# Kernel optimization log

Measured on AMD Instinct MI355X. Metric: run time of the kernel, lower is better.

## Reference

```python
import jax, jax.numpy as jnp
import numpy as np

D_MODEL = 272
D_STATE = 32
N_LAYERS = 12
D_INNER = 2 * D_MODEL      # expand=2 (mamba_ssm default)
D_CONV = 4                 # mamba_ssm default
DT_RANK = (D_MODEL + 15) // 16  # ceil(272/16) = 17
B_SZ = 2
SEQ = 512


def setup_inputs() -> dict:
    key = jax.random.key(0)
    ks = jax.random.split(key, 16)
    rn = lambda k, shape, s=0.02: jax.random.normal(k, shape, jnp.float32) * s
    # dt bias init: softplus^{-1} of dt in [1e-3, 0.1] (mamba-style)
    dt0 = jax.random.uniform(ks[6], (N_LAYERS, 2, D_INNER), jnp.float32, 1e-3, 0.1)
    a_log = jnp.broadcast_to(jnp.log(jnp.arange(1, D_STATE + 1, dtype=jnp.float32)),
                             (N_LAYERS, 2, D_INNER, D_STATE))
    return {
        "x": jax.random.normal(ks[0], (B_SZ, SEQ, D_MODEL), jnp.float32),
        "y": jax.random.uniform(ks[1], (B_SZ, 1), jnp.float32),
        "in_proj_w": rn(ks[2], (N_LAYERS, 2, 2 * D_INNER, D_MODEL)),
        "conv_w": rn(ks[3], (N_LAYERS, 2, D_INNER, D_CONV), 0.1),
        "conv_b": jnp.zeros((N_LAYERS, 2, D_INNER), jnp.float32),
        "x_proj_w": rn(ks[4], (N_LAYERS, 2, DT_RANK + 2 * D_STATE, D_INNER)),
        "dt_proj_w": rn(ks[5], (N_LAYERS, 2, D_INNER, DT_RANK), 0.1),
        "dt_proj_b": jnp.log(jnp.expm1(dt0)),
        "A_log": a_log,
        "Dskip": jnp.ones((N_LAYERS, 2, D_INNER), jnp.float32),
        "out_proj_w": rn(ks[7], (N_LAYERS, 2, D_MODEL, D_INNER)),
        "lambda_q1": rn(ks[8], (N_LAYERS, D_MODEL), 0.05),
        "norm1_w": jnp.ones((N_LAYERS, D_MODEL), jnp.float32),
        "norm2_w": jnp.ones((N_LAYERS, D_MODEL), jnp.float32),
        "mlp_w": rn(ks[9], (D_MODEL, D_MODEL)),
        "mlp_b": jnp.zeros((D_MODEL,), jnp.float32),
        "predict_w": rn(ks[10], (1, D_MODEL + 1)),
        "predict_b": jnp.zeros((1,), jnp.float32),
    }


def _rmsnorm(x, w, eps=1e-5):
    return x * jax.lax.rsqrt(jnp.mean(x * x, axis=-1, keepdims=True) + eps) * w


def _mamba(x, p):
    """Single-direction Mamba block. x: (B, L, D_MODEL)."""
    in_w, cw, cb, xw, dtw, dtb, a_log, dskip, ow = p
    bsz = x.shape[0]
    xz = jnp.einsum('bld,ed->ble', x, in_w)            # (B,L,2*D_INNER)
    xin, z = jnp.split(xz, 2, axis=-1)
    # causal depthwise conv1d, kernel 4
    xc = jax.lax.conv_general_dilated(
        xin.transpose(0, 2, 1), cw[:, None, :], (1,), [(D_CONV - 1, 0)],
        feature_group_count=D_INNER, dimension_numbers=('NCL', 'OIL', 'NCL'))
    xc = jax.nn.silu(xc + cb[:, None]).transpose(0, 2, 1)  # (B,L,D_INNER)
    dbc = jnp.einsum('bld,ed->ble', xc, xw)
    dt, Bm, Cm = jnp.split(dbc, [DT_RANK, DT_RANK + D_STATE], axis=-1)
    dt = jax.nn.softplus(jnp.einsum('blr,dr->bld', dt, dtw) + dtb)  # (B,L,D_INNER)
    A = -jnp.exp(a_log)                                  # (D_INNER, D_STATE)

    @jax.checkpoint
    def step(h, inp):
        dt_t, x_t, B_t, C_t = inp                        # (B,Din),(B,Din),(B,Ds),(B,Ds)
        h = jnp.exp(dt_t[..., None] * A) * h + (dt_t * x_t)[..., None] * B_t[:, None, :]
        return h, jnp.einsum('bds,bs->bd', h, C_t)

    h0 = jnp.zeros((bsz, D_INNER, D_STATE), x.dtype)
    xs = (dt.transpose(1, 0, 2), xc.transpose(1, 0, 2),
          Bm.transpose(1, 0, 2), Cm.transpose(1, 0, 2))
    _, ys = jax.lax.scan(step, h0, xs)                   # ys: (L,B,D_INNER)
    yo = ys.transpose(1, 0, 2) + dskip * xc
    yo = yo * jax.nn.silu(z)
    return jnp.einsum('bld,od->blo', yo, ow)


def _forward(x, y, in_proj_w, conv_w, conv_b, x_proj_w, dt_proj_w, dt_proj_b,
             A_log, Dskip, out_proj_w, lambda_q1, norm1_w, norm2_w,
             mlp_w, mlp_b, predict_w, predict_b):
    mats = (in_proj_w, conv_w, conv_b, x_proj_w, dt_proj_w, dt_proj_b, A_log, Dskip, out_proj_w)
    for i in range(N_LAYERS):
        lam_init = 0.8 - 0.6 * np.exp(-0.3 * i)
        xn = _rmsnorm(x, norm1_w[i])
        lam_full = jax.nn.sigmoid(jnp.sum(lambda_q1[i])) + lam_init
        y1 = _mamba(xn, tuple(a[i, 0] for a in mats))
        y2 = jnp.flip(_mamba(jnp.flip(xn, 1), tuple(a[i, 1] for a in mats)), 1)
        attn = _rmsnorm(y1 - lam_full * y2, norm2_w[i])
        x = x + attn * (1.0 - lam_init)
    x2 = jax.nn.relu(jnp.mean(x, axis=1) @ mlp_w.T + mlp_b)
    feats = jnp.concatenate([x2, y], axis=-1)
    logits = feats @ predict_w.T + predict_b
    return logits, x2


def reference(x, y, in_proj_w, conv_w, conv_b, x_proj_w, dt_proj_w, dt_proj_b,
              A_log, Dskip, out_proj_w, lambda_q1, norm1_w, norm2_w,
              mlp_w, mlp_b, predict_w, predict_b):
    return _forward(x, y, in_proj_w, conv_w, conv_b, x_proj_w, dt_proj_w, dt_proj_b,
                    A_log, Dskip, out_proj_w, lambda_q1, norm1_w, norm2_w,
                    mlp_w, mlp_b, predict_w, predict_b)
```

## Files before the change

kernel.cpp:

```cpp
#include <hip/hip_runtime.h>
#include <math.h>

#define DM   272
#define DS   32
#define DI   544
#define DTR  17
#define SEQL 512
#define NB   2
#define ROWS 1024
#define DXZ  1088
#define NL   12
#define KP   288

typedef unsigned short ushort_t;
typedef __attribute__((ext_vector_type(8))) short bx8;
typedef __attribute__((ext_vector_type(4))) float fx4;

#define OFF_X     0
#define OFF_XZ    279552
#define OFF_XCT   2507776
#define OFF_DTT   3621888
#define OFF_ZT    4736000
#define OFF_BM    5850112
#define OFF_CM    5915648
#define OFF_YOT   5981184
#define OFF_Y12   7095296
#define OFF_XMP   7652352
#define OFF_DTWT  7656704
#define OFF_XNH   7878656
#define OFF_XNL   8026112
#define OFF_WINH  8173568
#define OFF_WINL  11933696
#define OFF_WOUTH 15693824
#define OFF_WOUTL 17469440

#define NINW  (12*2176*KP)
#define NOUTW (12*544*544)

__device__ __forceinline__ float sigmoid_fast(float x){ return 1.f/(1.f+__expf(-x)); }
__device__ __forceinline__ float softplus_f(float x){ return (x > 20.f) ? x : log1pf(__expf(x)); }

__device__ __forceinline__ void bf16split(float x, ushort_t& h, ushort_t& l){
  unsigned uh = __float_as_uint(x) & 0xffff0000u;
  h = (ushort_t)(uh >> 16);
  float r = x - __uint_as_float(uh);
  l = (ushort_t)(__float_as_uint(r) >> 16);
}

__device__ __forceinline__ float block_reduce_256(float v, volatile float* sred, int tid){
#pragma unroll
  for (int m=32; m>=1; m>>=1) v += __shfl_xor(v, m);
  __syncthreads();
  if ((tid & 63) == 0) sred[tid>>6] = v;
  __syncthreads();
  return sred[0]+sred[1]+sred[2]+sred[3];
}

__global__ __launch_bounds__(256) void k_prep(
    const float* __restrict__ inw, const float* __restrict__ outw,
    const float* __restrict__ dtw, const float* __restrict__ x0,
    const float* __restrict__ n1w0,
    ushort_t* __restrict__ winh, ushort_t* __restrict__ winl,
    ushort_t* __restrict__ wouth, ushort_t* __restrict__ woutl,
    float* __restrict__ dtwT, float* __restrict__ xb,
    ushort_t* __restrict__ xnh, ushort_t* __restrict__ xnl)
{
  const int bid = blockIdx.x, tid = threadIdx.x;
  for (int idx = bid*256 + tid; idx < NINW + NOUTW; idx += 1024*256){
    if (idx < NINW){
      int k = idx % KP; int row = idx / KP;
      float v = (k < DM) ? inw[(size_t)row*DM + k] : 0.f;
      ushort_t h,l; bf16split(v,h,l);
      winh[idx]=h; winl[idx]=l;
    } else {
      int j = idx - NINW;
      float v = outw[j];
      ushort_t h,l; bf16split(v,h,l);
      wouth[j]=h; woutl[j]=l;
    }
  }
  for (int idx = bid*256 + tid; idx < 24*544*DTR; idx += 1024*256){
    int ld = idx / (544*DTR); int rem = idx - ld*(544*DTR);
    int d = rem / DTR; int r = rem - d*DTR;
    dtwT[(size_t)ld*DTR*544 + (size_t)r*544 + d] = dtw[idx];
  }
  if (tid < 64){
    const int r = bid, l = tid;
    float vv[5]; float ss = 0.f;
#pragma unroll
    for (int i=0;i<5;i++){
      int c = l + i*64; float v = 0.f;
      if (c < DM){ v = x0[(size_t)r*DM+c]; xb[(size_t)r*DM+c]=v; }
      vv[i]=v; ss += v*v;
    }
#pragma unroll
    for (int m=32;m>=1;m>>=1) ss += __shfl_xor(ss,m);
    float ivr = rsqrtf(ss*(1.f/DM)+1e-5f);
#pragma unroll
    for (int i=0;i<5;i++){
      int c = l + i*64;
      if (c < DM){
        ushort_t h,lo; bf16split(vv[i]*ivr*n1w0[c],h,lo);
        xnh[(size_t)r*KP+c]=h; xnl[(size_t)r*KP+c]=lo;
      }
    }
    if (l < 16){ xnh[(size_t)r*KP+DM+l]=0; xnl[(size_t)r*KP+DM+l]=0; }
  }
}

__global__ __launch_bounds__(256) void k_gin(
  const ushort_t* __restrict__ xnh, const ushort_t* __restrict__ xnl,
  const ushort_t* __restrict__ wh,  const ushort_t* __restrict__ wl,
  float* __restrict__ xz)
{
  const int tid = threadIdx.x;
  const int wv = tid >> 6, lane = tid & 63;
  const int m16 = lane & 15, quad = lane >> 4;
  const int q8 = quad << 3;
  const int m0 = blockIdx.x << 6;
  const int nt = blockIdx.y;
  const int dir = (nt >= 17) ? 1 : 0;
  const int n0l = (nt - dir*17) << 6;
  const int ncol = n0l + (wv<<4) + m16;
  const ushort_t* bhp = wh + (size_t)(dir*1088 + ncol)*KP + q8;
  const ushort_t* blp = wl + (size_t)(dir*1088 + ncol)*KP + q8;
  const ushort_t* ahp = xnh + (size_t)(m0 + m16)*KP + q8;
  const ushort_t* alp = xnl + (size_t)(m0 + m16)*KP + q8;
  fx4 acc[4];
#pragma unroll
  for (int mt=0;mt<4;mt++) acc[mt] = (fx4){0.f,0.f,0.f,0.f};
  for (int k0=0;k0<KP;k0+=32){
    bx8 bh = *(const bx8*)(bhp + k0);
    bx8 bl = *(const bx8*)(blp + k0);
#pragma unroll
    for (int mt=0;mt<4;mt++){
      bx8 ah = *(const bx8*)(ahp + (size_t)mt*16*KP + k0);
      bx8 al = *(const bx8*)(alp + (size_t)mt*16*KP + k0);
      acc[mt] = __builtin_amdgcn_mfma_f32_16x16x32_bf16(ah, bh, acc[mt], 0,0,0);
      acc[mt] = __builtin_amdgcn_mfma_f32_16x16x32_bf16(al, bh, acc[mt], 0,0,0);
      acc[mt] = __builtin_amdgcn_mfma_f32_16x16x32_bf16(ah, bl, acc[mt], 0,0,0);
    }
  }
#pragma unroll
  for (int mt=0;mt<4;mt++){
#pragma unroll
    for (int r=0;r<4;r++){
      int rg = m0 + mt*16 + quad*4 + r;
      int b = rg >> 9, t = rg & 511;
      int ts = dir ? (511 - t) : t;
      xz[((size_t)((dir*NB + b)*SEQL + ts))*DXZ + ncol] = acc[mt][r];
    }
  }
}

__global__ __launch_bounds__(512) void k_xdt(
  const float* __restrict__ xz, const float* __restrict__ cwl, const float* __restrict__ cbl,
  const float* __restrict__ xwl, const float* __restrict__ dtwTl, const float* __restrict__ dtbl,
  float* __restrict__ xcT, float* __restrict__ dtT, float* __restrict__ zT,
  float* __restrict__ Bmg, float* __restrict__ Cmg)
{
  __shared__ float xcs[8][548];
  __shared__ float part[8][8][82];
  __shared__ float dts[8][DTR];
  const int tid = threadIdx.x;
  const int blk = blockIdx.x;
  const int seg = blk >> 6;
  const int dir = seg >> 1;
  const int t0 = (blk & 63) << 3;
  const float* xzb  = xz + (size_t)seg*SEQL*DXZ;
  const float* cw   = cwl + dir*DI*4;
  const float* cb   = cbl + dir*DI;
  const float* xw   = xwl + (size_t)dir*81*DI;
  const float* dtwT = dtwTl + (size_t)dir*DTR*DI;
  const float* dtb  = dtbl + dir*DI;
  const size_t chb = (size_t)seg*DI;

  for (int j = tid; j < DI; j += 512){
    float4 w4 = *(const float4*)(cw + j*4);
    float bj = cb[j];
    float xv[11];
#pragma unroll
    for (int q=0; q<11; q++){
      int t = t0 + q - 3;
      xv[q] = (t >= 0) ? xzb[(size_t)t*DXZ + j] : 0.f;
    }
    float xo[8], zo[8];
#pragma unroll
    for (int rr=0; rr<8; rr++){
      float acc = bj + w4.x*xv[rr] + w4.y*xv[rr+1] + w4.z*xv[rr+2] + w4.w*xv[rr+3];
      float v = acc * sigmoid_fast(acc);
      xcs[rr][j] = v; xo[rr] = v;
      zo[rr] = xzb[(size_t)(t0+rr)*DXZ + 544 + j];
    }
    float* xr = xcT + (chb + j)*SEQL + t0;
    *(float4*)(xr)   = make_float4(xo[0],xo[1],xo[2],xo[3]);
    *(float4*)(xr+4) = make_float4(xo[4],xo[5],xo[6],xo[7]);
    float* zr = zT + (chb + j)*SEQL + t0;
    *(float4*)(zr)   = make_float4(zo[0],zo[1],zo[2],zo[3]);
    *(float4*)(zr+4) = make_float4(zo[4],zo[5],zo[6],zo[7]);
  }
  __syncthreads();

  if (tid < 328){
    const int i = tid >> 3, ks = tid & 7;
    const int e0 = 2*i;
    const int e1r = (e0+1 < 81) ? (e0+1) : 80;
    const int kb = ks*68;
    const float* w0 = xw + (size_t)e0*DI + kb;
    const float* w1 = xw + (size_t)e1r*DI + kb;
    float acc0[8], acc1[8];
#pragma unroll
    for (int rr=0; rr<8; rr++){ acc0[rr]=0.f; acc1[rr]=0.f; }
    for (int k=0; k<68; k+=4){
      float4 wa = *(const float4*)(w0 + k);
      float4 wb = *(const float4*)(w1 + k);
#pragma unroll
      for (int rr=0; rr<8; rr++){
        float4 x4 = *(const float4*)(&xcs[rr][kb + k]);
        acc0[rr] = fmaf(wa.x,x4.x, fmaf(wa.y,x4.y, fmaf(wa.z,x4.z, fmaf(wa.w,x4.w, acc0[rr]))));
        acc1[rr] = fmaf(wb.x,x4.x, fmaf(wb.y,x4.y, fmaf(wb.z,x4.z, fmaf(wb.w,x4.w, acc1[rr]))));
      }
    }
#pragma unroll
    for (int rr=0; rr<8; rr++){
      part[ks][rr][e0]   = acc0[rr];
      part[ks][rr][e0+1] = acc1[rr];
    }
  }
  __syncthreads();

  for (int idx=tid; idx<648; idx+=512){
    int ta = idx / 81, e = idx - ta*81;
    float s = 0.f;
#pragma unroll
    for (int ks=0; ks<8; ks++) s += part[ks][ta][e];
    size_t row = (size_t)seg*SEQL + t0 + ta;
    if (e < DTR)      dts[ta][e] = s;
    else if (e < 49)  Bmg[row*DS + (e-DTR)] = s;
    else              Cmg[row*DS + (e-49)] = s;
  }
  __syncthreads();

  {
    const int c1 = tid;
    const bool h2 = tid < 32; const int c2 = 512 + tid;
    float w1[DTR], w2[DTR];
#pragma unroll
    for (int q=0; q<DTR; q++){
      w1[q] = dtwT[q*DI + c1];
      w2[q] = h2 ? dtwT[q*DI + c2] : 0.f;
    }
    float b1 = dtb[c1], b2 = h2 ? dtb[c2] : 0.f;
    float o1[8], o2[8];
#pragma unroll
    for (int rr=0; rr<8; rr++){
      float a1=b1, a2=b2;
#pragma unroll
      for (int q=0; q<DTR; q++){
        float dv = dts[rr][q];
        a1 = fmaf(w1[q],dv,a1); a2 = fmaf(w2[q],dv,a2);
      }
      o1[rr]=softplus_f(a1); o2[rr]=softplus_f(a2);
    }
    float* r1 = dtT + (chb + c1)*SEQL + t0;
    *(float4*)(r1)   = make_float4(o1[0],o1[1],o1[2],o1[3]);
    *(float4*)(r1+4) = make_float4(o1[4],o1[5],o1[6],o1[7]);
    if (h2){
      float* r2 = dtT + (chb + c2)*SEQL + t0;
      *(float4*)(r2)   = make_float4(o2[0],o2[1],o2[2],o2[3]);
      *(float4*)(r2+4) = make_float4(o2[4],o2[5],o2[6],o2[7]);
    }
  }
}

__global__ __launch_bounds__(128) void k_scan(
  const float* __restrict__ dtT, const float* __restrict__ xcT,
  const float* __restrict__ Bmg, const float* __restrict__ Cmg,
  const float* __restrict__ alogl, const float* __restrict__ dskl,
  const float* __restrict__ zT, float* __restrict__ yoT)
{
  __shared__ float hl[16][33], pl[16][33], Hi[16][33];
  const int d = blockIdx.x, b = blockIdx.y, dir = blockIdx.z;
  const int seg = dir*NB + b;
  const int tid = threadIdx.x;
  const int c = tid >> 3, sg = tid & 7, s0 = sg << 2;
  float A0,A1,A2,A3;
  {
    const float* al = alogl + (size_t)(dir*DI + d)*DS + s0;
    A0 = -expf(al[0]); A1 = -expf(al[1]); A2 = -expf(al[2]); A3 = -expf(al[3]);
  }
  const size_t cr = ((size_t)seg*DI + d)*SEQL;
  const float* dtr = dtT + cr;
  const float* xcr = xcT + cr;
  const float* zr  = zT  + cr;
  float* yor = yoT + cr;
  const float* Bp = Bmg + (size_t)seg*SEQL*DS + s0;
  const float* Cp = Cmg + (size_t)seg*SEQL*DS + s0;
  float h0=0,h1=0,h2=0,h3=0,p0=1,p1=1,p2=1,p3=1;
  const int tb = c << 5;
  for (int tq=0; tq<8; tq++){
    const int t4 = tb + (tq<<2);
    float4 dt4 = *(const float4*)(dtr + t4);
    const float* dtp4 = (const float*)&dt4;
    float4 xc4 = *(const float4*)(xcr + t4);
    const float* xcp4 = (const float*)&xc4;
#pragma unroll
    for (int u=0; u<4; u++){
      float ldt = dtp4[u], lxc = xcp4[u];
      float4 B4 = *(const float4*)(Bp + (size_t)(t4+u)*DS);
      float uu = ldt*lxc;
      float e;
      e = __expf(ldt*A0); h0 = fmaf(e,h0,uu*B4.x); p0*=e;
      e = __expf(ldt*A1); h1 = fmaf(e,h1,uu*B4.y); p1*=e;
      e = __expf(ldt*A2); h2 = fmaf(e,h2,uu*B4.z); p2*=e;
      e = __expf(ldt*A3); h3 = fmaf(e,h3,uu*B4.w); p3*=e;
    }
  }
  hl[c][s0]=h0; hl[c][s0+1]=h1; hl[c][s0+2]=h2; hl[c][s0+3]=h3;
  pl[c][s0]=p0; pl[c][s0+1]=p1; pl[c][s0+2]=p2; pl[c][s0+3]=p3;
  __syncthreads();
  if (tid < 32){
    float H = 0.f;
    Hi[0][tid] = 0.f;
    for (int cc=1; cc<16; cc++){
      H = fmaf(pl[cc-1][tid], H, hl[cc-1][tid]);
      Hi[cc][tid] = H;
    }
  }
  __syncthreads();
  h0=Hi[c][s0]; h1=Hi[c][s0+1]; h2=Hi[c][s0+2]; h3=Hi[c][s0+3];
  const float dsk = dskl[dir*DI + d];
  for (int tq=0; tq<8; tq++){
    const int t4 = tb + (tq<<2);
    float4 dt4 = *(const float4*)(dtr + t4);
    const float* dtp4 = (const float*)&dt4;
    float4 xc4 = *(const float4*)(xcr + t4);
    const float* xcp4 = (const float*)&xc4;
    float4 z4 = *(const float4*)(zr + t4);
    const float* zp4 = (const float*)&z4;
    float yv[4];
#pragma unroll
    for (int u=0; u<4; u++){
      float ldt = dtp4[u], lxc = xcp4[u];
      float4 B4 = *(const float4*)(Bp + (size_t)(t4+u)*DS);
      float4 C4 = *(const float4*)(Cp + (size_t)(t4+u)*DS);
      float uu = ldt*lxc;
      float e;
      e = __expf(ldt*A0); h0 = fmaf(e,h0,uu*B4.x);
      e = __expf(ldt*A1); h1 = fmaf(e,h1,uu*B4.y);
      e = __expf(ldt*A2); h2 = fmaf(e,h2,uu*B4.z);
      e = __expf(ldt*A3); h3 = fmaf(e,h3,uu*B4.w);
      float y = h0*C4.x + h1*C4.y + h2*C4.z + h3*C4.w;
      y += __shfl_xor(y,1); y += __shfl_xor(y,2); y += __shfl_xor(y,4);
      float z = zp4[u];
      yv[u] = fmaf(dsk, lxc, y) * (z * sigmoid_fast(z));
    }
    if (sg==0) *(float4*)(yor + t4) = make_float4(yv[0],yv[1],yv[2],yv[3]);
  }
}

__global__ __launch_bounds__(256) void k_gout2(
  const float* __restrict__ yoT,
  const ushort_t* __restrict__ wh, const ushort_t* __restrict__ wl,
  float* __restrict__ y12)
{
  __shared__ ushort_t ash[64][72];
  __shared__ ushort_t asl[64][72];
  const int tid = threadIdx.x;
  const int wv = tid >> 6, lane = tid & 63;
  const int m16 = lane & 15, quad = lane >> 4, q8 = quad << 3;
  const int m0 = blockIdx.x << 6;
  const int n0 = blockIdx.y << 6;
  const int dir = blockIdx.z;
  const int seg = dir*NB + (m0 >> 9);
  const int t0 = m0 & 511;
  const int nloc = n0 + (wv<<4) + m16;
  const bool nval = nloc < DM;
  const int nrow = dir*DM + (nval ? nloc : 0);
  const ushort_t* bhp = wh + (size_t)nrow*DI + q8;
  const ushort_t* blp = wl + (size_t)nrow*DI + q8;
  const int tt = tid & 63;
  const int kq = tid >> 6;
  const float* yob = yoT + (size_t)seg*DI*SEQL + t0 + tt;
  fx4 acc[4];
#pragma unroll
  for (int mt=0;mt<4;mt++) acc[mt] = (fx4){0.f,0.f,0.f,0.f};

  float vbuf[8];
#pragma unroll
  for (int i=0;i<8;i++) vbuf[i] = yob[(size_t)(kq*8 + i)*SEQL];

  for (int k0=0; k0<DI; k0+=32){
    ushort_t h8[8], l8[8];
#pragma unroll
    for (int i=0;i<8;i++) bf16split(vbuf[i], h8[i], l8[i]);
    uint4 ph, pl;
    ph.x = (unsigned)h8[0] | ((unsigned)h8[1]<<16);
    ph.y = (unsigned)h8[2] | ((unsigned)h8[3]<<16);
    ph.z = (unsigned)h8[4] | ((unsigned)h8[5]<<16);
    ph.w = (unsigned)h8[6] | ((unsigned)h8[7]<<16);
    pl.x = (unsigned)l8[0] | ((unsigned)l8[1]<<16);
    pl.y = (unsigned)l8[2] | ((unsigned)l8[3]<<16);
    pl.z = (unsigned)l8[4] | ((unsigned)l8[5]<<16);
    pl.w = (unsigned)l8[6] | ((unsigned)l8[7]<<16);
    __syncthreads();
    *(uint4*)(&ash[tt][kq*8]) = ph;
    *(uint4*)(&asl[tt][kq*8]) = pl;
    __syncthreads();
    if (k0 + 32 < DI){
#pragma unroll
      for (int i=0;i<8;i++) vbuf[i] = yob[(size_t)(k0 + 32 + kq*8 + i)*SEQL];
    }
    bx8 bh = *(const bx8*)(bhp + k0);
    bx8 bl = *(const bx8*)(blp + k0);
#pragma unroll
    for (int mt=0;mt<4;mt++){
      bx8 ah = *(const bx8*)(&ash[mt*16 + m16][q8]);
      bx8 al = *(const bx8*)(&asl[mt*16 + m16][q8]);
      acc[mt] = __builtin_amdgcn_mfma_f32_16x16x32_bf16(ah, bh, acc[mt], 0,0,0);
      acc[mt] = __builtin_amdgcn_mfma_f32_16x16x32_bf16(al, bh, acc[mt], 0,0,0);
      acc[mt] = __builtin_amdgcn_mfma_f32_16x16x32_bf16(ah, bl, acc[mt], 0,0,0);
    }
  }
  if (nval){
#pragma unroll
    for (int mt=0;mt<4;mt++){
#pragma unroll
      for (int r=0;r<4;r++){
        int rg = m0 + mt*16 + quad*4 + r;
        int b = rg >> 9, t = rg & 511;
        int ts = dir ? (511 - t) : t;
        y12[(size_t)dir*ROWS*DM + ((size_t)(b*SEQL + ts))*DM + nloc] = acc[mt][r];
      }
    }
  }
}

__global__ __launch_bounds__(256) void k_combine(
  const float* __restrict__ y12, const float* __restrict__ lamq,
  const float* __restrict__ n2w, float* __restrict__ xb,
  const float* __restrict__ n1wn, ushort_t* __restrict__ xnh, ushort_t* __restrict__ xnl,
  float lam_init, float omli)
{
  __shared__ float sred[4];
  const int tid = threadIdx.x;
  const int r = blockIdx.x;
  const float* y1 = y12 + (size_t)r*DM;
  const float* y2 = y12 + (size_t)ROWS*DM + (size_t)r*DM;
  float lp = lamq[tid];
  if (tid < 16) lp += lamq[tid+256];
  float lsum = block_reduce_256(lp, sred, tid);
  float lam = sigmoid_fast(lsum) + lam_init;
  float a0 = y1[tid] - lam*y2[tid];
  float a1 = 0.f;
  if (tid<16) a1 = y1[tid+256] - lam*y2[tid+256];
  float ss = block_reduce_256(a0*a0 + a1*a1, sred, tid);
  float rms = rsqrtf(ss*(1.f/DM) + 1e-5f);
  float xo0 = xb[(size_t)r*DM + tid] + a0*rms*n2w[tid]*omli;
  float xo1 = 0.f;
  if (tid<16) xo1 = xb[(size_t)r*DM + tid+256] + a1*rms*n2w[tid+256]*omli;
  xb[(size_t)r*DM+tid] = xo0;
  if (tid<16) xb[(size_t)r*DM+tid+256] = xo1;
  float ss2 = block_reduce_256(xo0*xo0 + xo1*xo1, sred, tid);
  float ivn = rsqrtf(ss2*(1.f/DM) + 1e-5f);
  {
    ushort_t h,l; bf16split(xo0*ivn*n1wn[tid], h, l);
    xnh[(size_t)r*KP + tid] = h; xnl[(size_t)r*KP + tid] = l;
  }
  if (tid < 16){
    ushort_t h,l; bf16split(xo1*ivn*n1wn[tid+256], h, l);
    xnh[(size_t)r*KP + tid+256] = h; xnl[(size_t)r*KP + tid+256] = l;
    xnh[(size_t)r*KP + DM + tid] = 0; xnl[(size_t)r*KP + DM + tid] = 0;
  }
}

__global__ __launch_bounds__(256) void k_head1(const float* __restrict__ xb, float* __restrict__ xmp){
  int ch = blockIdx.x, b = blockIdx.y, tid = threadIdx.x;
  int t0 = ch*64;
  float s0=0.f, s1=0.f;
  for (int t=t0; t<t0+64; t++){
    const float* row = xb + (size_t)(b*SEQL+t)*DM;
    s0 += row[tid];
    if (tid<16) s1 += row[tid+256];
  }
  xmp[(size_t)(b*8+ch)*DM + tid] = s0;
  if (tid<16) xmp[(size_t)(b*8+ch)*DM + tid+256] = s1;
}

__global__ __launch_bounds__(256) void k_head2(
  const float* __restrict__ xmp, const float* __restrict__ yin,
  const float* __restrict__ mlpw, const float* __restrict__ mlpb,
  const float* __restrict__ pw, const float* __restrict__ pb,
  float* __restrict__ out)
{
  __shared__ float xm[2][DM];
  __shared__ float x2s[2][DM];
  __shared__ float sred[4];
  int tid = threadIdx.x;
  for (int idx=tid; idx<2*DM; idx+=256){
    int b = idx / DM, c = idx - b*DM;
    float s=0.f;
    for (int ch=0; ch<8; ch++) s += xmp[(size_t)(b*8+ch)*DM + c];
    xm[b][c] = s * (1.f/SEQL);
  }
  __syncthreads();
  for (int idx=tid; idx<2*DM; idx+=256){
    int b = idx / DM, c = idx - b*DM;
    float acc = mlpb[c];
    const float* wr = mlpw + (size_t)c*DM;
    for (int k=0;k<DM;k++) acc += wr[k]*xm[b][k];
    float v = fmaxf(acc, 0.f);
    x2s[b][c] = v;
    out[2 + b*DM + c] = v;
  }
  __syncthreads();
  for (int b=0;b<2;b++){
    float p = x2s[b][tid]*pw[tid];
    if (tid<16) p += x2s[b][tid+256]*pw[tid+256];
    float tot = block_reduce_256(p, sred, tid);
    if (tid==0) out[b] = tot + yin[b]*pw[DM] + pb[0];
  }
}

extern "C" void kernel_launch(void* const* d_in, const int* in_sizes, int n_in,
                              void* d_out, int out_size, void* d_ws, size_t ws_size,
                              hipStream_t stream)
{
  const float* x0     = (const float*)d_in[0];
  const float* yin    = (const float*)d_in[1];
  const float* in_w   = (const float*)d_in[2];
  const float* conv_w = (const float*)d_in[3];
  const float* conv_b = (const float*)d_in[4];
  const float* x_w    = (const float*)d_in[5];
  const float* dt_w   = (const float*)d_in[6];
  const float* dt_b   = (const float*)d_in[7];
  const float* a_log  = (const float*)d_in[8];
  const float* dskip  = (const float*)d_in[9];
  const float* out_w  = (const float*)d_in[10];
  const float* lamq   = (const float*)d_in[11];
  const float* n1w    = (const float*)d_in[12];
  const float* n2w    = (const float*)d_in[13];
  const float* mlpw   = (const float*)d_in[14];
  const float* mlpb   = (const float*)d_in[15];
  const float* pw     = (const float*)d_in[16];
  const float* pb     = (const float*)d_in[17];

  float* ws  = (float*)d_ws;
  float* xb  = ws + OFF_X;
  float* xz  = ws + OFF_XZ;
  float* xcT = ws + OFF_XCT;
  float* dtT = ws + OFF_DTT;
  float* zT  = ws + OFF_ZT;
  float* Bm  = ws + OFF_BM;
  float* Cm  = ws + OFF_CM;
  float* yoT = ws + OFF_YOT;
  float* y12 = ws + OFF_Y12;
  float* xmp = ws + OFF_XMP;
  float* dtwT= ws + OFF_DTWT;
  ushort_t* xnh  = (ushort_t*)(ws + OFF_XNH);
  ushort_t* xnl  = (ushort_t*)(ws + OFF_XNL);
  ushort_t* winh = (ushort_t*)(ws + OFF_WINH);
  ushort_t* winl = (ushort_t*)(ws + OFF_WINL);
  ushort_t* wouth= (ushort_t*)(ws + OFF_WOUTH);
  ushort_t* woutl= (ushort_t*)(ws + OFF_WOUTL);
  float* outp = (float*)d_out;

  k_prep<<<1024, 256, 0, stream>>>(in_w, out_w, dt_w, x0, n1w,
      winh, winl, wouth, woutl, dtwT, xb, xnh, xnl);
  for (int i=0;i<NL;i++){
    float lam_init = 0.8f - 0.6f*expf(-0.3f*(float)i);
    k_gin<<<dim3(16,34), 256, 0, stream>>>(xnh, xnl,
        winh + (size_t)i*2176*KP, winl + (size_t)i*2176*KP, xz);
    k_xdt<<<256, 512, 0, stream>>>(xz,
        conv_w + (size_t)i*2*DI*4, conv_b + (size_t)i*2*DI,
        x_w + (size_t)i*2*81*DI, dtwT + (size_t)i*2*DTR*DI, dt_b + (size_t)i*2*DI,
        xcT, dtT, zT, Bm, Cm);
    k_scan<<<dim3(DI,NB,2), 128, 0, stream>>>(dtT, xcT, Bm, Cm,
        a_log + (size_t)i*2*DI*DS, dskip + (size_t)i*2*DI, zT, yoT);
    k_gout2<<<dim3(16,5,2), 256, 0, stream>>>(yoT,
        wouth + (size_t)i*544*544, woutl + (size_t)i*544*544, y12);
    k_combine<<<ROWS, 256, 0, stream>>>(y12, lamq + (size_t)i*DM, n2w + (size_t)i*DM,
        xb, n1w + (size_t)((i+1)%NL)*DM, xnh, xnl, lam_init, 1.f - lam_init);
  }
  k_head1<<<dim3(8,2), 256, 0, stream>>>(xb, xmp);
  k_head2<<<1, 256, 0, stream>>>(xmp, yin, mlpw, mlpb, pw, pb, outp);
}
```

Measured before the change: 1.377 ms.

## Emit bf16 hi/lo split from scan in row-major layout, drop LDS staging in out-proj GEMM

The scan kernel now splits its output into bf16 high/low parts itself and writes them in token-major (row, channel) layout, with eight lanes each storing one scalar. The out-projection GEMM then reads its A operand straight from global memory as 8-element vectors, dropping the shared-memory transpose, conversion and both barriers per k-step. The scan's stores become scattered 2-byte writes with stride DI, and the GEMM gives up LDS reuse of the A tile across its four waves.

```diff
diff --git a/kernel.cpp b/kernel.cpp
--- a/kernel.cpp
+++ b/kernel.cpp
@@ -23,7 +23,8 @@
 #define OFF_ZT    4736000
 #define OFF_BM    5850112
 #define OFF_CM    5915648
-#define OFF_YOT   5981184
+#define OFF_YTMH  5981184
+#define OFF_YTML  6538240
 #define OFF_Y12   7095296
 #define OFF_XMP   7652352
 #define OFF_DTWT  7656704
@@ -277,7 +278,8 @@
   const float* __restrict__ dtT, const float* __restrict__ xcT,
   const float* __restrict__ Bmg, const float* __restrict__ Cmg,
   const float* __restrict__ alogl, const float* __restrict__ dskl,
-  const float* __restrict__ zT, float* __restrict__ yoT)
+  const float* __restrict__ zT,
+  ushort_t* __restrict__ ytmh, ushort_t* __restrict__ ytml)
 {
   __shared__ float hl[16][33], pl[16][33], Hi[16][33];
   const int d = blockIdx.x, b = blockIdx.y, dir = blockIdx.z;
@@ -293,7 +295,6 @@
   const float* dtr = dtT + cr;
   const float* xcr = xcT + cr;
   const float* zr  = zT  + cr;
-  float* yor = yoT + cr;
   const float* Bp = Bmg + (size_t)seg*SEQL*DS + s0;
   const float* Cp = Cmg + (size_t)seg*SEQL*DS + s0;
   float h0=0,h1=0,h2=0,h3=0,p0=1,p1=1,p2=1,p3=1;
@@ -330,6 +331,8 @@
   __syncthreads();
   h0=Hi[c][s0]; h1=Hi[c][s0+1]; h2=Hi[c][s0+2]; h3=Hi[c][s0+3];
   const float dsk = dskl[dir*DI + d];
+  const int uo = sg & 3;
+  ushort_t* ybase = (sg >= 4) ? ytml : ytmh;
   for (int tq=0; tq<8; tq++){
     const int t4 = tb + (tq<<2);
     float4 dt4 = *(const float4*)(dtr + t4);
@@ -355,68 +358,42 @@
       float z = zp4[u];
       yv[u] = fmaf(dsk, lxc, y) * (z * sigmoid_fast(z));
     }
-    if (sg==0) *(float4*)(yor + t4) = make_float4(yv[0],yv[1],yv[2],yv[3]);
-  }
-}
-
-__global__ __launch_bounds__(256) void k_gout2(
-  const float* __restrict__ yoT,
-  const ushort_t* __restrict__ wh, const ushort_t* __restrict__ wl,
+    ushort_t hh, ll; bf16split(yv[uo], hh, ll);
+    ybase[((size_t)(seg*SEQL + t4 + uo))*DI + d] = (sg >= 4) ? ll : hh;
+  }
+}
+
+__global__ __launch_bounds__(256) void k_gout(
+  const ushort_t* __restrict__ ath, const ushort_t* __restrict__ atl,
+  const ushort_t* __restrict__ wh,  const ushort_t* __restrict__ wl,
   float* __restrict__ y12)
 {
-  __shared__ ushort_t ash[64][72];
-  __shared__ ushort_t asl[64][72];
   const int tid = threadIdx.x;
   const int wv = tid >> 6, lane = tid & 63;
-  const int m16 = lane & 15, quad = lane >> 4, q8 = quad << 3;
+  const int m16 = lane & 15, quad = lane >> 4;
+  const int q8 = quad << 3;
   const int m0 = blockIdx.x << 6;
-  const int n0 = blockIdx.y << 6;
   const int dir = blockIdx.z;
-  const int seg = dir*NB + (m0 >> 9);
-  const int t0 = m0 & 511;
-  const int nloc = n0 + (wv<<4) + m16;
+  const int nloc = (blockIdx.y << 6) + (wv<<4) + m16;
   const bool nval = nloc < DM;
-  const int nrow = dir*DM + (nval ? nloc : 0);
+  const int nrow = dir*DM + (nval ? nloc : (DM-1));
+  const int bseg = m0 >> 9;
+  const int tr0 = m0 & 511;
+  const int seg = dir*NB + bseg;
   const ushort_t* bhp = wh + (size_t)nrow*DI + q8;
   const ushort_t* blp = wl + (size_t)nrow*DI + q8;
-  const int tt = tid & 63;
-  const int kq = tid >> 6;
-  const float* yob = yoT + (size_t)seg*DI*SEQL + t0 + tt;
+  const ushort_t* ahp = ath + ((size_t)(seg*SEQL) + tr0 + m16)*DI + q8;
+  const ushort_t* alp = atl + ((size_t)(seg*SEQL) + tr0 + m16)*DI + q8;
   fx4 acc[4];
 #pragma unroll
   for (int mt=0;mt<4;mt++) acc[mt] = (fx4){0.f,0.f,0.f,0.f};
-
-  float vbuf[8];
-#pragma unroll
-  for (int i=0;i<8;i++) vbuf[i] = yob[(size_t)(kq*8 + i)*SEQL];
-
-  for (int k0=0; k0<DI; k0+=32){
-    ushort_t h8[8], l8[8];
-#pragma unroll
-    for (int i=0;i<8;i++) bf16split(vbuf[i], h8[i], l8[i]);
-    uint4 ph, pl;
-    ph.x = (unsigned)h8[0] | ((unsigned)h8[1]<<16);
-    ph.y = (unsigned)h8[2] | ((unsigned)h8[3]<<16);
-    ph.z = (unsigned)h8[4] | ((unsigned)h8[5]<<16);
-    ph.w = (unsigned)h8[6] | ((unsigned)h8[7]<<16);
-    pl.x = (unsigned)l8[0] | ((unsigned)l8[1]<<16);
-    pl.y = (unsigned)l8[2] | ((unsigned)l8[3]<<16);
-    pl.z = (unsigned)l8[4] | ((unsigned)l8[5]<<16);
-    pl.w = (unsigned)l8[6] | ((unsigned)l8[7]<<16);
-    __syncthreads();
-    *(uint4*)(&ash[tt][kq*8]) = ph;
-    *(uint4*)(&asl[tt][kq*8]) = pl;
-    __syncthreads();
-    if (k0 + 32 < DI){
-#pragma unroll
-      for (int i=0;i<8;i++) vbuf[i] = yob[(size_t)(k0 + 32 + kq*8 + i)*SEQL];
-    }
+  for (int k0=0;k0<DI;k0+=32){
     bx8 bh = *(const bx8*)(bhp + k0);
     bx8 bl = *(const bx8*)(blp + k0);
 #pragma unroll
     for (int mt=0;mt<4;mt++){
-      bx8 ah = *(const bx8*)(&ash[mt*16 + m16][q8]);
-      bx8 al = *(const bx8*)(&asl[mt*16 + m16][q8]);
+      bx8 ah = *(const bx8*)(ahp + (size_t)mt*16*DI + k0);
+      bx8 al = *(const bx8*)(alp + (size_t)mt*16*DI + k0);
       acc[mt] = __builtin_amdgcn_mfma_f32_16x16x32_bf16(ah, bh, acc[mt], 0,0,0);
       acc[mt] = __builtin_amdgcn_mfma_f32_16x16x32_bf16(al, bh, acc[mt], 0,0,0);
       acc[mt] = __builtin_amdgcn_mfma_f32_16x16x32_bf16(ah, bl, acc[mt], 0,0,0);
@@ -553,10 +530,11 @@
   float* zT  = ws + OFF_ZT;
   float* Bm  = ws + OFF_BM;
   float* Cm  = ws + OFF_CM;
-  float* yoT = ws + OFF_YOT;
   float* y12 = ws + OFF_Y12;
   float* xmp = ws + OFF_XMP;
   float* dtwT= ws + OFF_DTWT;
+  ushort_t* ytmh = (ushort_t*)(ws + OFF_YTMH);
+  ushort_t* ytml = (ushort_t*)(ws + OFF_YTML);
   ushort_t* xnh  = (ushort_t*)(ws + OFF_XNH);
   ushort_t* xnl  = (ushort_t*)(ws + OFF_XNL);
   ushort_t* winh = (ushort_t*)(ws + OFF_WINH);
@@ -576,8 +554,8 @@
         x_w + (size_t)i*2*81*DI, dtwT + (size_t)i*2*DTR*DI, dt_b + (size_t)i*2*DI,
         xcT, dtT, zT, Bm, Cm);
     k_scan<<<dim3(DI,NB,2), 128, 0, stream>>>(dtT, xcT, Bm, Cm,
-        a_log + (size_t)i*2*DI*DS, dskip + (size_t)i*2*DI, zT, yoT);
-    k_gout2<<<dim3(16,5,2), 256, 0, stream>>>(yoT,
+        a_log + (size_t)i*2*DI*DS, dskip + (size_t)i*2*DI, zT, ytmh, ytml);
+    k_gout<<<dim3(16,5,2), 256, 0, stream>>>(ytmh, ytml,
         wouth + (size_t)i*544*544, woutl + (size_t)i*544*544, y12);
     k_combine<<<ROWS, 256, 0, stream>>>(y12, lamq + (size_t)i*DM, n2w + (size_t)i*DM,
         xb, n1w + (size_t)((i+1)%NL)*DM, xnh, xnl, lam_init, 1.f - lam_init);
```

Result: slower. 1.417 ms (+2.9%).
